# Kernel tuning notes

Hardware: AMD Instinct MI355X
Metric: run time of the kernel (lower is better)

Reference implementation:

```python
import jax, jax.numpy as jnp
import numpy as np

VOCAB, EMB, CLASSES = 100000, 128, 1000
B, L = 16384, 200


def setup_inputs() -> dict:
    key = jax.random.key(0)
    k1, k2, k3, k4 = jax.random.split(key, 4)
    seq = jax.random.randint(k1, (B, L), 0, VOCAB, dtype=jnp.int64) if jax.config.jax_enable_x64 else jax.random.randint(k1, (B, L), 0, VOCAB).astype(jnp.int32)
    emb_table = jax.random.normal(k2, (VOCAB, EMB), dtype=jnp.float32) * 0.02
    fc_w = jax.random.normal(k3, (CLASSES, EMB), dtype=jnp.float32) * 0.02
    fc_b = jax.random.normal(k4, (CLASSES,), dtype=jnp.float32) * 0.02
    return {"seq": seq, "emb_table": emb_table, "fc_w": fc_w, "fc_b": fc_b}


def reference(seq, emb_table, fc_w, fc_b):
    # Masked embedding-bag (sum pool): tokens with id 0 are padding and excluded,
    # exactly matching the original nonzero-gather-sum loop.
    mask = (seq != 0).astype(emb_table.dtype)          # [B, L]
    gathered = emb_table[seq]                          # [B, L, E]
    pooled = jnp.einsum("ble,bl->be", gathered, mask)  # [B, E] sum over valid tokens
    return pooled @ fc_w.T + fc_b                      # [B, C]
```

## Files before the change

kernel.cpp:

```cpp
#include <hip/hip_runtime.h>

#define VOCAB   100000
#define EMB     128
#define CLASSES 1000
#define BATCH   16384
#define SEQLEN  200

typedef short bf16x8 __attribute__((ext_vector_type(8)));
typedef float f32x4  __attribute__((ext_vector_type(4)));

__device__ __forceinline__ unsigned short f32_to_bf16(float f) {
    unsigned int u = __builtin_bit_cast(unsigned int, f);
    u += 0x7fffu + ((u >> 16) & 1u);
    return (unsigned short)(u >> 16);
}
__device__ __forceinline__ float bf_lo(unsigned int p) { return __builtin_bit_cast(float, p << 16); }
__device__ __forceinline__ float bf_hi(unsigned int p) { return __builtin_bit_cast(float, p & 0xffff0000u); }
__device__ __forceinline__ float sb(unsigned int w, int sh) {
    return (float)(int)(signed char)((w >> sh) & 0xffu);
}

__global__ __launch_bounds__(256) void convert_emb_i8(const float* __restrict__ emb,
                                                      const float* __restrict__ fcw,
                                                      unsigned char* __restrict__ e8,
                                                      float* __restrict__ scl,
                                                      unsigned short* __restrict__ wb) {
    if (blockIdx.x < 6250) {
        const int row = blockIdx.x * 16 + (threadIdx.x >> 4);
        const int c8  = (threadIdx.x & 15) * 8;
        const float* r = emb + (long)row * EMB + c8;
        float4 v0 = *(const float4*)(r);
        float4 v1 = *(const float4*)(r + 4);
        float m = fmaxf(fmaxf(fmaxf(fabsf(v0.x), fabsf(v0.y)), fmaxf(fabsf(v0.z), fabsf(v0.w))),
                        fmaxf(fmaxf(fabsf(v1.x), fabsf(v1.y)), fmaxf(fabsf(v1.z), fabsf(v1.w))));
        m = fmaxf(m, __shfl_xor(m, 1));
        m = fmaxf(m, __shfl_xor(m, 2));
        m = fmaxf(m, __shfl_xor(m, 4));
        m = fmaxf(m, __shfl_xor(m, 8));
        const float inv = (m > 0.f) ? 127.0f / m : 0.f;
#define Q(x) ((int)fminf(fmaxf(__builtin_rintf((x) * inv), -127.f), 127.f))
        int q0 = Q(v0.x), q1 = Q(v0.y), q2 = Q(v0.z), q3 = Q(v0.w);
        int q4 = Q(v1.x), q5 = Q(v1.y), q6 = Q(v1.z), q7 = Q(v1.w);
#undef Q
        uint2 o;
        o.x = (unsigned int)(q0 & 255) | ((unsigned int)(q1 & 255) << 8) |
              ((unsigned int)(q2 & 255) << 16) | ((unsigned int)(q3 & 255) << 24);
        o.y = (unsigned int)(q4 & 255) | ((unsigned int)(q5 & 255) << 8) |
              ((unsigned int)(q6 & 255) << 16) | ((unsigned int)(q7 & 255) << 24);
        *(uint2*)(e8 + (long)row * EMB + c8) = o;
        if ((threadIdx.x & 15) == 0) scl[row] = m * (1.0f / 127.0f);
    } else {
        long i = (((long)blockIdx.x - 6250) * 256 + threadIdx.x) * 8;
        if (i >= (long)CLASSES * EMB) return;
        float4 v0 = *(const float4*)(fcw + i);
        float4 v1 = *(const float4*)(fcw + i + 4);
        uint4 o;
        o.x = (unsigned int)f32_to_bf16(v0.x) | ((unsigned int)f32_to_bf16(v0.y) << 16);
        o.y = (unsigned int)f32_to_bf16(v0.z) | ((unsigned int)f32_to_bf16(v0.w) << 16);
        o.z = (unsigned int)f32_to_bf16(v1.x) | ((unsigned int)f32_to_bf16(v1.y) << 16);
        o.w = (unsigned int)f32_to_bf16(v1.z) | ((unsigned int)f32_to_bf16(v1.w) << 16);
        *(uint4*)(wb + i) = o;
    }
}

__global__ __launch_bounds__(1024, 4) void pool_gemm_i8(const int* __restrict__ seq,
                                                        const unsigned char* __restrict__ e8,
                                                        const float* __restrict__ scl,
                                                        const unsigned short* __restrict__ fcw,
                                                        const float* __restrict__ fcb,
                                                        float* __restrict__ out) {
    __shared__ unsigned short Asub[64][136];

    const int lane = threadIdx.x & 63;
    const int wid  = threadIdx.x >> 6;
    const int quad = lane >> 4;
    const int dsub = (lane & 15) * 8;
    const int bbase = blockIdx.x * 64;

#define ISSUE(IDS, G, T, U, S)                                                \
    T = __shfl((IDS), 4 * (G) + quad);                                        \
    U = *(const uint2*)(e8 + (long)T * EMB + dsub);                           \
    S = scl[T];
#define ACCUM(T, U, S)                                                        \
    {                                                                         \
        float ms = (T != 0) ? S : 0.0f;                                       \
        a0 += ms * sb(U.x, 0);  a1 += ms * sb(U.x, 8);                        \
        a2 += ms * sb(U.x, 16); a3 += ms * sb(U.x, 24);                       \
        a4 += ms * sb(U.y, 0);  a5 += ms * sb(U.y, 8);                        \
        a6 += ms * sb(U.y, 16); a7 += ms * sb(U.y, 24);                       \
    }
#define PIPE8(IDS, G0)                                                        \
    {                                                                         \
        int t0, t1, t2, t3, t4, t5, t6, t7;                                   \
        uint2 u0, u1, u2, u3, u4, u5, u6, u7;                                 \
        float s0, s1, s2, s3, s4, s5, s6, s7;                                 \
        ISSUE(IDS, (G0) + 0, t0, u0, s0)                                      \
        ISSUE(IDS, (G0) + 1, t1, u1, s1)                                      \
        ISSUE(IDS, (G0) + 2, t2, u2, s2)                                      \
        ISSUE(IDS, (G0) + 3, t3, u3, s3)                                      \
        ISSUE(IDS, (G0) + 4, t4, u4, s4)                                      \
        ISSUE(IDS, (G0) + 5, t5, u5, s5)                                      \
        ISSUE(IDS, (G0) + 6, t6, u6, s6)                                      \
        ISSUE(IDS, (G0) + 7, t7, u7, s7)                                      \
        ACCUM(t0, u0, s0) ACCUM(t1, u1, s1) ACCUM(t2, u2, s2) ACCUM(t3, u3, s3) \
        ACCUM(t4, u4, s4) ACCUM(t5, u5, s5) ACCUM(t6, u6, s6) ACCUM(t7, u7, s7) \
    }

#pragma unroll 1
    for (int j = 0; j < 4; ++j) {
        const int bagLocal = wid * 4 + j;
        const int* srow = seq + (long)(bbase + bagLocal) * SEQLEN;
        int ids0 = srow[lane];
        int ids1 = srow[lane + 64];
        int ids2 = srow[lane + 128];
        int ids3 = (lane < 8) ? srow[lane + 192] : 0;

        float a0 = 0.f, a1 = 0.f, a2 = 0.f, a3 = 0.f;
        float a4 = 0.f, a5 = 0.f, a6 = 0.f, a7 = 0.f;

        PIPE8(ids0, 0)
        PIPE8(ids0, 8)
        PIPE8(ids1, 0)
        PIPE8(ids1, 8)
        PIPE8(ids2, 0)
        PIPE8(ids2, 8)
        {
            int t0, t1;
            uint2 u0, u1;
            float s0, s1;
            ISSUE(ids3, 0, t0, u0, s0)
            ISSUE(ids3, 1, t1, u1, s1)
            ACCUM(t0, u0, s0) ACCUM(t1, u1, s1)
        }

        a0 += __shfl_xor(a0, 16); a1 += __shfl_xor(a1, 16);
        a2 += __shfl_xor(a2, 16); a3 += __shfl_xor(a3, 16);
        a4 += __shfl_xor(a4, 16); a5 += __shfl_xor(a5, 16);
        a6 += __shfl_xor(a6, 16); a7 += __shfl_xor(a7, 16);
        a0 += __shfl_xor(a0, 32); a1 += __shfl_xor(a1, 32);
        a2 += __shfl_xor(a2, 32); a3 += __shfl_xor(a3, 32);
        a4 += __shfl_xor(a4, 32); a5 += __shfl_xor(a5, 32);
        a6 += __shfl_xor(a6, 32); a7 += __shfl_xor(a7, 32);

        if (lane < 16) {
            uint4 o;
            o.x = (unsigned int)f32_to_bf16(a0) | ((unsigned int)f32_to_bf16(a1) << 16);
            o.y = (unsigned int)f32_to_bf16(a2) | ((unsigned int)f32_to_bf16(a3) << 16);
            o.z = (unsigned int)f32_to_bf16(a4) | ((unsigned int)f32_to_bf16(a5) << 16);
            o.w = (unsigned int)f32_to_bf16(a6) | ((unsigned int)f32_to_bf16(a7) << 16);
            *(uint4*)(&Asub[bagLocal][dsub]) = o;
        }
    }
#undef PIPE8
#undef ACCUM
#undef ISSUE

    __syncthreads();

    const int arow = lane & 15;
    const int koff = quad * 8;
#define LDA(Aa, ROWOFF)                                                        \
    bf16x8 Aa##0 = *(const bf16x8*)(&Asub[(ROWOFF) + arow][koff + 0]);         \
    bf16x8 Aa##1 = *(const bf16x8*)(&Asub[(ROWOFF) + arow][koff + 32]);        \
    bf16x8 Aa##2 = *(const bf16x8*)(&Asub[(ROWOFF) + arow][koff + 64]);        \
    bf16x8 Aa##3 = *(const bf16x8*)(&Asub[(ROWOFF) + arow][koff + 96]);
    LDA(A0_, 0) LDA(A1_, 16) LDA(A2_, 32) LDA(A3_, 48)
#undef LDA

    int t = wid;
    int cc = t * 16 + (lane & 15);
    const unsigned short* wr = fcw + (long)((cc < CLASSES) ? cc : 0) * EMB + koff;
    bf16x8 w0 = *(const bf16x8*)(wr + 0 * 32);
    bf16x8 w1 = *(const bf16x8*)(wr + 1 * 32);
    bf16x8 w2 = *(const bf16x8*)(wr + 2 * 32);
    bf16x8 w3 = *(const bf16x8*)(wr + 3 * 32);

#pragma unroll 1
    while (t < 63) {
        bf16x8 c0 = w0, c1 = w1, c2 = w2, c3 = w3;
        const int ccNow = cc;
        t += 16;
        if (t < 63) {
            cc = t * 16 + (lane & 15);
            const unsigned short* wn = fcw + (long)((cc < CLASSES) ? cc : 0) * EMB + koff;
            w0 = *(const bf16x8*)(wn + 0 * 32);
            w1 = *(const bf16x8*)(wn + 1 * 32);
            w2 = *(const bf16x8*)(wn + 2 * 32);
            w3 = *(const bf16x8*)(wn + 3 * 32);
        }
        f32x4 acc0 = {0.f, 0.f, 0.f, 0.f};
        f32x4 acc1 = {0.f, 0.f, 0.f, 0.f};
        f32x4 acc2 = {0.f, 0.f, 0.f, 0.f};
        f32x4 acc3 = {0.f, 0.f, 0.f, 0.f};
        acc0 = __builtin_amdgcn_mfma_f32_16x16x32_bf16(A0_0, c0, acc0, 0, 0, 0);
        acc1 = __builtin_amdgcn_mfma_f32_16x16x32_bf16(A1_0, c0, acc1, 0, 0, 0);
        acc2 = __builtin_amdgcn_mfma_f32_16x16x32_bf16(A2_0, c0, acc2, 0, 0, 0);
        acc3 = __builtin_amdgcn_mfma_f32_16x16x32_bf16(A3_0, c0, acc3, 0, 0, 0);
        acc0 = __builtin_amdgcn_mfma_f32_16x16x32_bf16(A0_1, c1, acc0, 0, 0, 0);
        acc1 = __builtin_amdgcn_mfma_f32_16x16x32_bf16(A1_1, c1, acc1, 0, 0, 0);
        acc2 = __builtin_amdgcn_mfma_f32_16x16x32_bf16(A2_1, c1, acc2, 0, 0, 0);
        acc3 = __builtin_amdgcn_mfma_f32_16x16x32_bf16(A3_1, c1, acc3, 0, 0, 0);
        acc0 = __builtin_amdgcn_mfma_f32_16x16x32_bf16(A0_2, c2, acc0, 0, 0, 0);
        acc1 = __builtin_amdgcn_mfma_f32_16x16x32_bf16(A1_2, c2, acc1, 0, 0, 0);
        acc2 = __builtin_amdgcn_mfma_f32_16x16x32_bf16(A2_2, c2, acc2, 0, 0, 0);
        acc3 = __builtin_amdgcn_mfma_f32_16x16x32_bf16(A3_2, c2, acc3, 0, 0, 0);
        acc0 = __builtin_amdgcn_mfma_f32_16x16x32_bf16(A0_3, c3, acc0, 0, 0, 0);
        acc1 = __builtin_amdgcn_mfma_f32_16x16x32_bf16(A1_3, c3, acc1, 0, 0, 0);
        acc2 = __builtin_amdgcn_mfma_f32_16x16x32_bf16(A2_3, c3, acc2, 0, 0, 0);
        acc3 = __builtin_amdgcn_mfma_f32_16x16x32_bf16(A3_3, c3, acc3, 0, 0, 0);

        if (ccNow < CLASSES) {
            const float bias = fcb[ccNow];
            float* orow0 = out + (long)(bbase +  0 + quad * 4) * CLASSES + ccNow;
            float* orow1 = out + (long)(bbase + 16 + quad * 4) * CLASSES + ccNow;
            float* orow2 = out + (long)(bbase + 32 + quad * 4) * CLASSES + ccNow;
            float* orow3 = out + (long)(bbase + 48 + quad * 4) * CLASSES + ccNow;
#pragma unroll
            for (int r = 0; r < 4; ++r) {
                orow0[(long)r * CLASSES] = acc0[r] + bias;
                orow1[(long)r * CLASSES] = acc1[r] + bias;
                orow2[(long)r * CLASSES] = acc2[r] + bias;
                orow3[(long)r * CLASSES] = acc3[r] + bias;
            }
        }
    }
}

__global__ __launch_bounds__(256) void convert_fcw(const float* __restrict__ fcw,
                                                   unsigned short* __restrict__ wb) {
    long i = ((long)blockIdx.x * 256 + threadIdx.x) * 8;
    if (i >= (long)CLASSES * EMB) return;
    float4 v0 = *(const float4*)(fcw + i);
    float4 v1 = *(const float4*)(fcw + i + 4);
    uint4 o;
    o.x = (unsigned int)f32_to_bf16(v0.x) | ((unsigned int)f32_to_bf16(v0.y) << 16);
    o.y = (unsigned int)f32_to_bf16(v0.z) | ((unsigned int)f32_to_bf16(v0.w) << 16);
    o.z = (unsigned int)f32_to_bf16(v1.x) | ((unsigned int)f32_to_bf16(v1.y) << 16);
    o.w = (unsigned int)f32_to_bf16(v1.z) | ((unsigned int)f32_to_bf16(v1.w) << 16);
    *(uint4*)(wb + i) = o;
}

__global__ __launch_bounds__(256) void bag_pool_f32(const int* __restrict__ seq,
                                                    const float* __restrict__ emb,
                                                    unsigned short* __restrict__ pooled) {
    const int lane = threadIdx.x & 63;
    const int wid  = threadIdx.x >> 6;
    const int b    = blockIdx.x * 4 + wid;
    const int* srow = seq + (long)b * SEQLEN;
    int ids0 = srow[lane];
    int ids1 = srow[lane + 64];
    int ids2 = srow[lane + 128];
    int ids3 = (lane < 8) ? srow[lane + 192] : 0;
    const int half = lane >> 5;
    const int dsub = (lane & 31) * 4;
    float4 acc = {0.f, 0.f, 0.f, 0.f};
#define PAIR_BODY(IDS, Q)                                                   \
    {                                                                       \
        int tok = __shfl((IDS), 2 * (Q) + half);                            \
        if (tok != 0) {                                                     \
            float4 v = *(const float4*)(emb + (long)tok * EMB + dsub);      \
            acc.x += v.x; acc.y += v.y; acc.z += v.z; acc.w += v.w;         \
        }                                                                   \
    }
#pragma unroll 8
    for (int q = 0; q < 32; ++q) PAIR_BODY(ids0, q)
#pragma unroll 8
    for (int q = 0; q < 32; ++q) PAIR_BODY(ids1, q)
#pragma unroll 8
    for (int q = 0; q < 32; ++q) PAIR_BODY(ids2, q)
#pragma unroll
    for (int q = 0; q < 4; ++q)  PAIR_BODY(ids3, q)
#undef PAIR_BODY
    acc.x += __shfl_xor(acc.x, 32);
    acc.y += __shfl_xor(acc.y, 32);
    acc.z += __shfl_xor(acc.z, 32);
    acc.w += __shfl_xor(acc.w, 32);
    if (lane < 32) {
        uint2 o;
        o.x = (unsigned int)f32_to_bf16(acc.x) | ((unsigned int)f32_to_bf16(acc.y) << 16);
        o.y = (unsigned int)f32_to_bf16(acc.z) | ((unsigned int)f32_to_bf16(acc.w) << 16);
        *(uint2*)(pooled + (long)b * EMB + dsub) = o;
    }
}

__global__ __launch_bounds__(256) void bow_gemm(const unsigned short* __restrict__ pooled,
                                                const unsigned short* __restrict__ fcw,
                                                const float* __restrict__ fcb,
                                                float* __restrict__ out) {
    const int lane = threadIdx.x & 63;
    const int wid  = threadIdx.x >> 6;
    const int quad = lane >> 4;
    const int m0   = blockIdx.x * 64 + wid * 16;
    const int mrow = m0 + (lane & 15);
    const int koff = quad * 8;

    const unsigned short* ar = pooled + (long)mrow * EMB + koff;
    bf16x8 a0 = *(const bf16x8*)(ar + 0 * 32);
    bf16x8 a1 = *(const bf16x8*)(ar + 1 * 32);
    bf16x8 a2 = *(const bf16x8*)(ar + 2 * 32);
    bf16x8 a3 = *(const bf16x8*)(ar + 3 * 32);

    int ccur = (blockIdx.y * 21) * 16 + (lane & 15);
    const unsigned short* wr = fcw + (long)((ccur < CLASSES) ? ccur : 0) * EMB + koff;
    bf16x8 w0 = *(const bf16x8*)(wr + 0 * 32);
    bf16x8 w1 = *(const bf16x8*)(wr + 1 * 32);
    bf16x8 w2 = *(const bf16x8*)(wr + 2 * 32);
    bf16x8 w3 = *(const bf16x8*)(wr + 3 * 32);

#pragma unroll 1
    for (int i = 0; i < 21; ++i) {
        bf16x8 c0 = w0, c1 = w1, c2 = w2, c3 = w3;
        const int cc = ccur;
        if (i + 1 < 21) {
            ccur += 16;
            const unsigned short* wn = fcw + (long)((ccur < CLASSES) ? ccur : 0) * EMB + koff;
            w0 = *(const bf16x8*)(wn + 0 * 32);
            w1 = *(const bf16x8*)(wn + 1 * 32);
            w2 = *(const bf16x8*)(wn + 2 * 32);
            w3 = *(const bf16x8*)(wn + 3 * 32);
        }
        f32x4 acc = {0.f, 0.f, 0.f, 0.f};
        acc = __builtin_amdgcn_mfma_f32_16x16x32_bf16(a0, c0, acc, 0, 0, 0);
        acc = __builtin_amdgcn_mfma_f32_16x16x32_bf16(a1, c1, acc, 0, 0, 0);
        acc = __builtin_amdgcn_mfma_f32_16x16x32_bf16(a2, c2, acc, 0, 0, 0);
        acc = __builtin_amdgcn_mfma_f32_16x16x32_bf16(a3, c3, acc, 0, 0, 0);

        if (cc < CLASSES) {
            const float bias = fcb[cc];
            float* orow = out + (long)(m0 + quad * 4) * CLASSES + cc;
#pragma unroll
            for (int r = 0; r < 4; ++r)
                orow[(long)r * CLASSES] = acc[r] + bias;
        }
    }
}

extern "C" void kernel_launch(void* const* d_in, const int* in_sizes, int n_in,
                              void* d_out, int out_size, void* d_ws, size_t ws_size,
                              hipStream_t stream) {
    const int*   seq = (const int*)d_in[0];
    const float* emb = (const float*)d_in[1];
    const float* fcw = (const float*)d_in[2];
    const float* fcb = (const float*)d_in[3];
    float*       out = (float*)d_out;

    float*          scl      = (float*)d_ws;
    unsigned char*  e8       = (unsigned char*)(scl + VOCAB);
    unsigned short* fcw_bf16 = (unsigned short*)(e8 + (long)VOCAB * EMB);

    const size_t need = (size_t)VOCAB * 4 + (size_t)VOCAB * EMB + (size_t)CLASSES * EMB * 2;

    if (ws_size >= need) {
        convert_emb_i8<<<6313, 256, 0, stream>>>(emb, fcw, e8, scl, fcw_bf16);
        pool_gemm_i8<<<BATCH / 64, 1024, 0, stream>>>(seq, e8, scl, fcw_bf16, fcb, out);
    } else {
        unsigned short* pooled  = (unsigned short*)d_ws;
        unsigned short* fcw_bf  = pooled + (long)BATCH * EMB;
        convert_fcw<<<63, 256, 0, stream>>>(fcw, fcw_bf);
        bag_pool_f32<<<BATCH / 4, 256, 0, stream>>>(seq, emb, pooled);
        bow_gemm<<<dim3(BATCH / 64, 3), 256, 0, stream>>>(pooled, fcw_bf, fcb, out);
    }
}
```

Measured before the change: 169.5 us.

## Partition embedding gather into three vocab ranges for cache locality

Measured after the change: 318.3 us. 1.88x slower.

```diff
diff --git a/kernel.cpp b/kernel.cpp
--- a/kernel.cpp
+++ b/kernel.cpp
@@ -77,62 +77,52 @@
     const int dsub = (lane & 15) * 8;
     const int bbase = blockIdx.x * 64;
 
-#define ISSUE(IDS, G, T, U, S)                                                \
-    T = __shfl((IDS), 4 * (G) + quad);                                        \
-    U = *(const uint2*)(e8 + (long)T * EMB + dsub);                           \
-    S = scl[T];
-#define ACCUM(T, U, S)                                                        \
+    float acc[4][8];
+#pragma unroll
+    for (int j = 0; j < 4; ++j)
+#pragma unroll
+        for (int k = 0; k < 8; ++k) acc[j][k] = 0.f;
+
+#define GATH(IDS, G)                                                          \
     {                                                                         \
-        float ms = (T != 0) ? S : 0.0f;                                       \
-        a0 += ms * sb(U.x, 0);  a1 += ms * sb(U.x, 8);                        \
-        a2 += ms * sb(U.x, 16); a3 += ms * sb(U.x, 24);                       \
-        a4 += ms * sb(U.y, 0);  a5 += ms * sb(U.y, 8);                        \
-        a6 += ms * sb(U.y, 16); a7 += ms * sb(U.y, 24);                       \
-    }
-#define PIPE8(IDS, G0)                                                        \
-    {                                                                         \
-        int t0, t1, t2, t3, t4, t5, t6, t7;                                   \
-        uint2 u0, u1, u2, u3, u4, u5, u6, u7;                                 \
-        float s0, s1, s2, s3, s4, s5, s6, s7;                                 \
-        ISSUE(IDS, (G0) + 0, t0, u0, s0)                                      \
-        ISSUE(IDS, (G0) + 1, t1, u1, s1)                                      \
-        ISSUE(IDS, (G0) + 2, t2, u2, s2)                                      \
-        ISSUE(IDS, (G0) + 3, t3, u3, s3)                                      \
-        ISSUE(IDS, (G0) + 4, t4, u4, s4)                                      \
-        ISSUE(IDS, (G0) + 5, t5, u5, s5)                                      \
-        ISSUE(IDS, (G0) + 6, t6, u6, s6)                                      \
-        ISSUE(IDS, (G0) + 7, t7, u7, s7)                                      \
-        ACCUM(t0, u0, s0) ACCUM(t1, u1, s1) ACCUM(t2, u2, s2) ACCUM(t3, u3, s3) \
-        ACCUM(t4, u4, s4) ACCUM(t5, u5, s5) ACCUM(t6, u6, s6) ACCUM(t7, u7, s7) \
+        int tk = __shfl((IDS), 4 * (G) + quad);                               \
+        if (tk >= lo && tk < hi) {                                            \
+            uint2 u = *(const uint2*)(e8 + (long)tk * EMB + dsub);            \
+            float ms = (tk != 0) ? scl[tk] : 0.0f;                            \
+            acc[j][0] += ms * sb(u.x, 0);  acc[j][1] += ms * sb(u.x, 8);      \
+            acc[j][2] += ms * sb(u.x, 16); acc[j][3] += ms * sb(u.x, 24);     \
+            acc[j][4] += ms * sb(u.y, 0);  acc[j][5] += ms * sb(u.y, 8);      \
+            acc[j][6] += ms * sb(u.y, 16); acc[j][7] += ms * sb(u.y, 24);     \
+        }                                                                     \
     }
 
 #pragma unroll 1
+    for (int p = 0; p < 3; ++p) {
+        const int lo = p * 33334;
+        const int hi = lo + 33334;
+#pragma unroll
+        for (int j = 0; j < 4; ++j) {
+            const int* srow = seq + (long)(bbase + wid * 4 + j) * SEQLEN;
+            int ids0 = srow[lane];
+            int ids1 = srow[lane + 64];
+            int ids2 = srow[lane + 128];
+            int ids3 = (lane < 8) ? srow[lane + 192] : 0;
+#pragma unroll
+            for (int g = 0; g < 16; ++g) GATH(ids0, g)
+#pragma unroll
+            for (int g = 0; g < 16; ++g) GATH(ids1, g)
+#pragma unroll
+            for (int g = 0; g < 16; ++g) GATH(ids2, g)
+#pragma unroll
+            for (int g = 0; g < 2; ++g)  GATH(ids3, g)
+        }
+    }
+#undef GATH
+
+#pragma unroll
     for (int j = 0; j < 4; ++j) {
-        const int bagLocal = wid * 4 + j;
-        const int* srow = seq + (long)(bbase + bagLocal) * SEQLEN;
-        int ids0 = srow[lane];
-        int ids1 = srow[lane + 64];
-        int ids2 = srow[lane + 128];
-        int ids3 = (lane < 8) ? srow[lane + 192] : 0;
-
-        float a0 = 0.f, a1 = 0.f, a2 = 0.f, a3 = 0.f;
-        float a4 = 0.f, a5 = 0.f, a6 = 0.f, a7 = 0.f;
-
-        PIPE8(ids0, 0)
-        PIPE8(ids0, 8)
-        PIPE8(ids1, 0)
-        PIPE8(ids1, 8)
-        PIPE8(ids2, 0)
-        PIPE8(ids2, 8)
-        {
-            int t0, t1;
-            uint2 u0, u1;
-            float s0, s1;
-            ISSUE(ids3, 0, t0, u0, s0)
-            ISSUE(ids3, 1, t1, u1, s1)
-            ACCUM(t0, u0, s0) ACCUM(t1, u1, s1)
-        }
-
+        float a0 = acc[j][0], a1 = acc[j][1], a2 = acc[j][2], a3 = acc[j][3];
+        float a4 = acc[j][4], a5 = acc[j][5], a6 = acc[j][6], a7 = acc[j][7];
         a0 += __shfl_xor(a0, 16); a1 += __shfl_xor(a1, 16);
         a2 += __shfl_xor(a2, 16); a3 += __shfl_xor(a3, 16);
         a4 += __shfl_xor(a4, 16); a5 += __shfl_xor(a5, 16);
@@ -141,19 +131,15 @@
         a2 += __shfl_xor(a2, 32); a3 += __shfl_xor(a3, 32);
         a4 += __shfl_xor(a4, 32); a5 += __shfl_xor(a5, 32);
         a6 += __shfl_xor(a6, 32); a7 += __shfl_xor(a7, 32);
-
         if (lane < 16) {
             uint4 o;
             o.x = (unsigned int)f32_to_bf16(a0) | ((unsigned int)f32_to_bf16(a1) << 16);
             o.y = (unsigned int)f32_to_bf16(a2) | ((unsigned int)f32_to_bf16(a3) << 16);
             o.z = (unsigned int)f32_to_bf16(a4) | ((unsigned int)f32_to_bf16(a5) << 16);
             o.w = (unsigned int)f32_to_bf16(a6) | ((unsigned int)f32_to_bf16(a7) << 16);
-            *(uint4*)(&Asub[bagLocal][dsub]) = o;
-        }
-    }
-#undef PIPE8
-#undef ACCUM
-#undef ISSUE
+            *(uint4*)(&Asub[wid * 4 + j][dsub]) = o;
+        }
+    }
 
     __syncthreads();
 
```
